# Kernel tuning notes

Measured on AMD Instinct MI355X. Metric: run time of the kernel, lower is better.

The kernel has to match this reference:

```python
import jax, jax.numpy as jnp
import numpy as np

# ROI Align config (module attributes in the original torch wrapper)
SPATIAL_SCALE = 0.25
POOLED_H = 7
POOLED_W = 7
SAMPLE_NUM = 2
ROI_END_MODE = 1  # Ascend: end coord gets +roi_end_mode before scaling


def setup_inputs() -> dict:
    key = jax.random.key(0)
    k_feat, k_b, k_xy, k_wh = jax.random.split(key, 4)
    B, C, H, W = 2, 256, 200, 200
    N = 1000
    feat = jax.random.normal(k_feat, (B, C, H, W), dtype=jnp.float32)
    img_h, img_w = H / SPATIAL_SCALE, W / SPATIAL_SCALE
    bidx = jax.random.randint(k_b, (N,), 0, B).astype(jnp.float32)
    xy = jax.random.uniform(k_xy, (N, 2), dtype=jnp.float32)
    wh = jax.random.uniform(k_wh, (N, 2), dtype=jnp.float32)
    x1 = xy[:, 0] * (img_w - 64.0)
    y1 = xy[:, 1] * (img_h - 64.0)
    x2 = x1 + 8.0 + wh[:, 0] * 200.0
    y2 = y1 + 8.0 + wh[:, 1] * 200.0
    rois = jnp.stack([bidx, x1, y1, x2, y2], axis=1)  # [N,5]
    return {"input": feat, "rois": rois}


def _axis_coords(start, bin_size, pooled, sn):
    # sample coord for grid index g: start + bin_size*(g+0.5)/sn, g in [0, pooled*sn)
    g = jnp.arange(pooled * sn, dtype=jnp.float32)
    return start[:, None] + bin_size[:, None] * (g[None, :] + 0.5) / sn  # [N, pooled*sn]


def _bilinear_1d(c, size):
    # returns (low_idx, high_idx, w_low, w_high, valid) for coordinate array c
    valid = (c >= -1.0) & (c <= size)
    cc = jnp.clip(c, 0.0, size - 1.0)
    lo = jnp.floor(cc).astype(jnp.int32)
    lo = jnp.clip(lo, 0, size - 1)
    hi = jnp.clip(lo + 1, 0, size - 1)
    frac = cc - lo.astype(jnp.float32)
    return lo, hi, 1.0 - frac, frac, valid


def roi_align(feat, rois):
    B, C, H, W = feat.shape
    N = rois.shape[0]
    bidx = rois[:, 0].astype(jnp.int32)
    off = float(ROI_END_MODE)
    x1 = rois[:, 1] * SPATIAL_SCALE
    y1 = rois[:, 2] * SPATIAL_SCALE
    x2 = (rois[:, 3] + off) * SPATIAL_SCALE
    y2 = (rois[:, 4] + off) * SPATIAL_SCALE
    roi_w = jnp.maximum(x2 - x1, 1.0)
    roi_h = jnp.maximum(y2 - y1, 1.0)
    bin_h = roi_h / POOLED_H
    bin_w = roi_w / POOLED_W

    ys = _axis_coords(y1, bin_h, POOLED_H, SAMPLE_NUM)  # [N, GY]
    xs = _axis_coords(x1, bin_w, POOLED_W, SAMPLE_NUM)  # [N, GX]
    yl, yh, wyl, wyh, vy = _bilinear_1d(ys, H)
    xl, xh, wxl, wxh, vx = _bilinear_1d(xs, W)

    b = bidx[:, None, None]

    def gather(yi, xi):
        # advanced indexing -> [N, GY, GX, C]
        return feat[b, :, yi[:, :, None], xi[:, None, :]]

    val = (wyl[:, :, None, None] * wxl[:, None, :, None] * gather(yl, xl)
           + wyl[:, :, None, None] * wxh[:, None, :, None] * gather(yl, xh)
           + wyh[:, :, None, None] * wxl[:, None, :, None] * gather(yh, xl)
           + wyh[:, :, None, None] * wxh[:, None, :, None] * gather(yh, xh))
    mask = (vy[:, :, None] & vx[:, None, :]).astype(val.dtype)[..., None]
    val = val * mask  # [N, GY, GX, C]

    # average pool over the SAMPLE_NUM x SAMPLE_NUM grid inside each bin
    val = val.reshape(N, POOLED_H, SAMPLE_NUM, POOLED_W, SAMPLE_NUM, C)
    out = val.mean(axis=(2, 4))  # [N, PH, PW, C]
    return jnp.transpose(out, (0, 3, 1, 2))  # [N, C, PH, PW]


def reference(input, rois):
    return roi_align(input, rois)
```

## Files before the change

kernel.cpp:

```cpp
#include <hip/hip_runtime.h>
#include <hip/hip_bf16.h>


constexpr int C_TOT  = 256;
constexpr int H_FEAT = 200;
constexpr int W_FEAT = 200;
constexpr int HW     = H_FEAT * W_FEAT;
constexpr int S_TOT  = 49;
constexpr size_t FEATT_BYTES = (size_t)2 * HW * C_TOT * sizeof(unsigned short);
constexpr int NXCD = 8;
constexpr int NBUCKET = 32;

__global__ __launch_bounds__(1024) void roi_bin_kernel(
    const float* __restrict__ rois, int* __restrict__ perm, int N)
{
    __shared__ int hist[NBUCKET];
    __shared__ int base[NBUCKET];
    __shared__ int cnt[NBUCKET];
    int t = threadIdx.x;

    if (t < NBUCKET) { hist[t] = 0; cnt[t] = 0; }
    __syncthreads();

    int bucket = -1;
    if (t < N) {
        const float* r = rois + (size_t)t * 5;
        int   b  = (int)r[0];
        float cx = (r[1] + r[3]) * 0.5f * 0.25f;
        float cy = (r[2] + r[4]) * 0.5f * 0.25f;
        int qx = min(max((int)(cx * (4.0f / 200.0f)), 0), 3);
        int qy = min(max((int)(cy * (4.0f / 200.0f)), 0), 3);
        bucket = ((b & 1) << 4) | (qy << 2) | qx;
        atomicAdd(&hist[bucket], 1);
    }
    __syncthreads();

    if (t == 0) {
        int acc = 0;
        for (int i = 0; i < NBUCKET; ++i) { base[i] = acc; acc += hist[i]; }
    }
    __syncthreads();

    if (t < N) {
        int pos = base[bucket] + atomicAdd(&cnt[bucket], 1);
        perm[pos] = t;
    }
}

__global__ __launch_bounds__(256) void nchw_to_nhwc_bf16_kernel(
    const float* __restrict__ feat,
    unsigned short* __restrict__ featT)
{
    __shared__ float tile[32][33];
    int tx = threadIdx.x;
    int ty = threadIdx.y;
    int s0 = blockIdx.x * 32;
    int c0 = blockIdx.y * 32;
    int b  = blockIdx.z;

    const float* src = feat + ((size_t)b * C_TOT) * HW;
    #pragma unroll
    for (int i = 0; i < 4; ++i) {
        int r = ty + i * 8;
        tile[r][tx] = src[(size_t)(c0 + r) * HW + (s0 + tx)];
    }
    __syncthreads();
    unsigned short* dst = featT + ((size_t)b * HW) * C_TOT;
    #pragma unroll
    for (int i = 0; i < 4; ++i) {
        int r = ty + i * 8;
        float x = tile[tx][r];
        unsigned int u = __float_as_uint(x);
        unsigned int rb = (u + 0x7fffu + ((u >> 16) & 1u)) >> 16;
        dst[(size_t)(s0 + r) * C_TOT + (c0 + tx)] = (unsigned short)rb;
    }
}

__global__ __launch_bounds__(512) void roi_align_nhwc_kernel(
    const unsigned short* __restrict__ featT,
    const float* __restrict__ rois,
    const int* __restrict__ perm,
    float* __restrict__ out,
    int N, int use_perm)
{
    __shared__ alignas(16) float tile[C_TOT * S_TOT];

    int n;
    if (use_perm) {
        int chunk = (N + NXCD - 1) / NXCD;
        int rank  = (blockIdx.x & (NXCD - 1)) * chunk + (blockIdx.x >> 3);
        if (rank >= N) rank = blockIdx.x;
        n = perm[rank];
    } else {
        n = blockIdx.x;
    }

    int tid  = threadIdx.x;
    int wave = tid >> 6;
    int lane = tid & 63;
    int half = lane >> 5;
    int li   = lane & 31;

    const float* r = rois + (size_t)n * 5;
    int   b  = (int)r[0];
    float x1 = r[1] * 0.25f;
    float y1 = r[2] * 0.25f;
    float x2 = (r[3] + 1.0f) * 0.25f;
    float y2 = (r[4] + 1.0f) * 0.25f;
    float bin_w = fmaxf(x2 - x1, 1.0f) * (1.0f / 7.0f);
    float bin_h = fmaxf(y2 - y1, 1.0f) * (1.0f / 7.0f);

    const unsigned short* fb = featT + (size_t)b * HW * C_TOT + li * 8;
    int xorsw = (li >> 2) & 7;

    for (int s = wave; s < S_TOT; s += 8) {
        int ph = s / 7;
        int pw = s - ph * 7;

        int   yoff[2][2];
        int   xoff[2][2];
        float wy[2][2], wx[2][2];
        #pragma unroll
        for (int i = 0; i < 2; ++i) {
            float gy  = (float)(2 * ph + i);
            float cy  = y1 + bin_h * ((gy + 0.5f) * 0.5f);
            bool  vy  = (cy >= -1.0f) && (cy <= (float)H_FEAT);
            float ccy = fminf(fmaxf(cy, 0.0f), (float)(H_FEAT - 1));
            int   ylo = (int)ccy;
            int   yhi = min(ylo + 1, H_FEAT - 1);
            float fy  = ccy - (float)ylo;
            yoff[i][0] = ylo * W_FEAT;
            yoff[i][1] = yhi * W_FEAT;
            wy[i][0] = vy ? (1.0f - fy) * 0.5f : 0.0f;
            wy[i][1] = vy ? fy * 0.5f          : 0.0f;

            float gx  = (float)(2 * pw + i);
            float cx  = x1 + bin_w * ((gx + 0.5f) * 0.5f);
            bool  vx  = (cx >= -1.0f) && (cx <= (float)W_FEAT);
            float ccx = fminf(fmaxf(cx, 0.0f), (float)(W_FEAT - 1));
            int   xlo = (int)ccx;
            int   xhi = min(xlo + 1, W_FEAT - 1);
            float fx  = ccx - (float)xlo;
            xoff[i][0] = xlo;
            xoff[i][1] = xhi;
            wx[i][0] = vx ? (1.0f - fx) * 0.5f : 0.0f;
            wx[i][1] = vx ? fx * 0.5f          : 0.0f;
        }

        float acc[8];
        #pragma unroll
        for (int j = 0; j < 8; ++j) acc[j] = 0.0f;

        #pragma unroll
        for (int iy = 0; iy < 2; ++iy)
        #pragma unroll
        for (int jy = 0; jy < 2; ++jy)
        #pragma unroll
        for (int ix = 0; ix < 2; ++ix) {
            int   pixA = yoff[iy][jy] + xoff[ix][0];
            int   pixB = yoff[iy][jy] + xoff[ix][1];
            float wA   = wy[iy][jy] * wx[ix][0];
            float wB   = wy[iy][jy] * wx[ix][1];
            int   pix  = half ? pixB : pixA;
            float w    = half ? wB   : wA;
            const uint4 v = *reinterpret_cast<const uint4*>(
                fb + (size_t)pix * C_TOT);
            unsigned int u;
            u = v.x;
            acc[0] = fmaf(w, __uint_as_float(u << 16),          acc[0]);
            acc[1] = fmaf(w, __uint_as_float(u & 0xffff0000u),  acc[1]);
            u = v.y;
            acc[2] = fmaf(w, __uint_as_float(u << 16),          acc[2]);
            acc[3] = fmaf(w, __uint_as_float(u & 0xffff0000u),  acc[3]);
            u = v.z;
            acc[4] = fmaf(w, __uint_as_float(u << 16),          acc[4]);
            acc[5] = fmaf(w, __uint_as_float(u & 0xffff0000u),  acc[5]);
            u = v.w;
            acc[6] = fmaf(w, __uint_as_float(u << 16),          acc[6]);
            acc[7] = fmaf(w, __uint_as_float(u & 0xffff0000u),  acc[7]);
        }

        #pragma unroll
        for (int j = 0; j < 8; ++j) {
            float sum = acc[j] + __shfl_xor(acc[j], 32);
            if (half == 0) {
                int slot_ch = li * 8 + (j ^ xorsw);
                tile[slot_ch * S_TOT + s] = sum;
            }
        }
    }
    __syncthreads();

    float4* o4 = reinterpret_cast<float4*>(out + (size_t)n * (C_TOT * S_TOT));
    constexpr int Q4 = C_TOT * S_TOT / 4;
    for (int q4 = tid; q4 < Q4; q4 += 512) {
        int q = q4 * 4;
        float4 val;
        float* vp = reinterpret_cast<float*>(&val);
        #pragma unroll
        for (int e = 0; e < 4; ++e) {
            int qq = q + e;
            int ch = qq / S_TOT;
            int ss = qq - ch * S_TOT;
            int slot_ch = (ch & ~7) | ((ch & 7) ^ ((ch >> 5) & 7));
            vp[e] = tile[slot_ch * S_TOT + ss];
        }
        o4[q4] = val;
    }
}

constexpr int CPT = 4;
constexpr int CG  = C_TOT / CPT;

__global__ __launch_bounds__(256) void roi_align_direct_kernel(
    const float* __restrict__ feat,
    const float* __restrict__ rois,
    float* __restrict__ out,
    int N)
{
    int t = blockIdx.x * 256 + threadIdx.x;
    int total = N * CG * S_TOT;
    if (t >= total) return;

    int s   = t % S_TOT;
    int rem = t / S_TOT;
    int c0  = rem % CG;
    int n   = rem / CG;
    int ph  = s / 7;
    int pw  = s - ph * 7;

    const float* r = rois + (size_t)n * 5;
    int   b  = (int)r[0];
    float x1 = r[1] * 0.25f;
    float y1 = r[2] * 0.25f;
    float x2 = (r[3] + 1.0f) * 0.25f;
    float y2 = (r[4] + 1.0f) * 0.25f;
    float bin_w = fmaxf(x2 - x1, 1.0f) * (1.0f / 7.0f);
    float bin_h = fmaxf(y2 - y1, 1.0f) * (1.0f / 7.0f);

    int   roff[2][2], coff[2][2];
    float wy[2][2], wx[2][2];
    #pragma unroll
    for (int i = 0; i < 2; ++i) {
        float gy  = (float)(2 * ph + i);
        float cy  = y1 + bin_h * ((gy + 0.5f) * 0.5f);
        bool  vy  = (cy >= -1.0f) && (cy <= (float)H_FEAT);
        float ccy = fminf(fmaxf(cy, 0.0f), (float)(H_FEAT - 1));
        int   ylo = (int)ccy;
        int   yhi = min(ylo + 1, H_FEAT - 1);
        float fy  = ccy - (float)ylo;
        roff[i][0] = ylo * W_FEAT;
        roff[i][1] = yhi * W_FEAT;
        wy[i][0] = vy ? (1.0f - fy) : 0.0f;
        wy[i][1] = vy ? fy          : 0.0f;

        float gx  = (float)(2 * pw + i);
        float cx  = x1 + bin_w * ((gx + 0.5f) * 0.5f);
        bool  vx  = (cx >= -1.0f) && (cx <= (float)W_FEAT);
        float ccx = fminf(fmaxf(cx, 0.0f), (float)(W_FEAT - 1));
        int   xlo = (int)ccx;
        int   xhi = min(xlo + 1, W_FEAT - 1);
        float fx  = ccx - (float)xlo;
        coff[i][0] = xlo;
        coff[i][1] = xhi;
        wx[i][0] = vx ? (1.0f - fx) : 0.0f;
        wx[i][1] = vx ? fx          : 0.0f;
    }

    float w16[16];
    int   o16[16];
    #pragma unroll
    for (int iy = 0; iy < 2; ++iy)
    #pragma unroll
    for (int ix = 0; ix < 2; ++ix)
    #pragma unroll
    for (int jy = 0; jy < 2; ++jy)
    #pragma unroll
    for (int jx = 0; jx < 2; ++jx) {
        int idx = ((iy * 2 + ix) * 2 + jy) * 2 + jx;
        w16[idx] = wy[iy][jy] * wx[ix][jx];
        o16[idx] = roff[iy][jy] + coff[ix][jx];
    }

    size_t base  = ((size_t)b * C_TOT + c0) * HW;
    size_t obase = (size_t)n * (C_TOT * S_TOT) + (size_t)c0 * S_TOT + s;

    #pragma unroll
    for (int k = 0; k < CPT; ++k) {
        const float* f = feat + base + (size_t)k * CG * HW;
        float acc = 0.0f;
        #pragma unroll
        for (int j = 0; j < 16; ++j)
            acc = fmaf(w16[j], f[o16[j]], acc);
        out[obase + (size_t)k * (CG * S_TOT)] = acc * 0.25f;
    }
}

extern "C" void kernel_launch(void* const* d_in, const int* in_sizes, int n_in,
                              void* d_out, int out_size, void* d_ws, size_t ws_size,
                              hipStream_t stream) {
    const float* feat = (const float*)d_in[0];
    const float* rois = (const float*)d_in[1];
    float* out = (float*)d_out;
    int N = in_sizes[1] / 5;

    size_t need = FEATT_BYTES + 4096;
    if (ws_size >= need) {
        unsigned short* featT = (unsigned short*)d_ws;
        int* perm = (int*)((char*)d_ws + FEATT_BYTES);
        int use_perm = (N <= 1024) ? 1 : 0;
        if (use_perm)
            roi_bin_kernel<<<1, 1024, 0, stream>>>(rois, perm, N);
        dim3 tgrid(HW / 32, C_TOT / 32, 2);
        dim3 tblk(32, 8);
        nchw_to_nhwc_bf16_kernel<<<tgrid, tblk, 0, stream>>>(feat, featT);
        roi_align_nhwc_kernel<<<N, 512, 0, stream>>>(featT, rois, perm, out, N, use_perm);
    } else {
        int total  = N * CG * S_TOT;
        int blocks = (total + 255) / 256;
        roi_align_direct_kernel<<<blocks, 256, 0, stream>>>(feat, rois, out, N);
    }
}
```

Before: 61.16 us.

## Use persistent ROI-align blocks pulling work from per-XCD atomic queues

Replaces the one-block-per-ROI launch with a persistent grid of up to 768 blocks. Each block reads its hardware XCD id and claims ROIs via atomic counters from per-XCD slices of the spatially sorted permutation, stealing from other XCDs once its own slice runs out. The bin ordering also changes to a Morton-like interleave so that ROIs sharing an XCD are spatially close, aiming for better L2 locality and load balance. In exchange it adds global atomics, an extra barrier per ROI, and a dependency on reading a hardware register for the XCD id.

```diff
diff --git a/kernel.cpp b/kernel.cpp
--- a/kernel.cpp
+++ b/kernel.cpp
@@ -10,9 +10,11 @@
 constexpr size_t FEATT_BYTES = (size_t)2 * HW * C_TOT * sizeof(unsigned short);
 constexpr int NXCD = 8;
 constexpr int NBUCKET = 32;
+#define XCC_GETREG_IMM 63508
 
 __global__ __launch_bounds__(1024) void roi_bin_kernel(
-    const float* __restrict__ rois, int* __restrict__ perm, int N)
+    const float* __restrict__ rois, int* __restrict__ perm,
+    int* __restrict__ qcnt, int N)
 {
     __shared__ int hist[NBUCKET];
     __shared__ int base[NBUCKET];
@@ -20,6 +22,7 @@
     int t = threadIdx.x;
 
     if (t < NBUCKET) { hist[t] = 0; cnt[t] = 0; }
+    if (t < NXCD + 1) qcnt[t] = 0;
     __syncthreads();
 
     int bucket = -1;
@@ -30,7 +33,8 @@
         float cy = (r[2] + r[4]) * 0.5f * 0.25f;
         int qx = min(max((int)(cx * (4.0f / 200.0f)), 0), 3);
         int qy = min(max((int)(cy * (4.0f / 200.0f)), 0), 3);
-        bucket = ((b & 1) << 4) | (qy << 2) | qx;
+        int m  = ((qy & 2) << 2) | ((qx & 2) << 1) | ((qy & 1) << 1) | (qx & 1);
+        bucket = ((b & 1) << 4) | m;
         atomicAdd(&hist[bucket], 1);
     }
     __syncthreads();
@@ -76,136 +80,151 @@
     }
 }
 
-__global__ __launch_bounds__(512) void roi_align_nhwc_kernel(
+__global__ __launch_bounds__(512) void roi_align_persistent_kernel(
     const unsigned short* __restrict__ featT,
     const float* __restrict__ rois,
     const int* __restrict__ perm,
+    int* __restrict__ qcnt,
     float* __restrict__ out,
-    int N, int use_perm)
+    int N)
 {
     __shared__ alignas(16) float tile[C_TOT * S_TOT];
-
-    int n;
-    if (use_perm) {
-        int chunk = (N + NXCD - 1) / NXCD;
-        int rank  = (blockIdx.x & (NXCD - 1)) * chunk + (blockIdx.x >> 3);
-        if (rank >= N) rank = blockIdx.x;
-        n = perm[rank];
-    } else {
-        n = blockIdx.x;
-    }
+    __shared__ int s_n;
 
     int tid  = threadIdx.x;
     int wave = tid >> 6;
     int lane = tid & 63;
     int half = lane >> 5;
     int li   = lane & 31;
-
-    const float* r = rois + (size_t)n * 5;
-    int   b  = (int)r[0];
-    float x1 = r[1] * 0.25f;
-    float y1 = r[2] * 0.25f;
-    float x2 = (r[3] + 1.0f) * 0.25f;
-    float y2 = (r[4] + 1.0f) * 0.25f;
-    float bin_w = fmaxf(x2 - x1, 1.0f) * (1.0f / 7.0f);
-    float bin_h = fmaxf(y2 - y1, 1.0f) * (1.0f / 7.0f);
-
-    const unsigned short* fb = featT + (size_t)b * HW * C_TOT + li * 8;
     int xorsw = (li >> 2) & 7;
 
-    for (int s = wave; s < S_TOT; s += 8) {
-        int ph = s / 7;
-        int pw = s - ph * 7;
-
-        int   yoff[2][2];
-        int   xoff[2][2];
-        float wy[2][2], wx[2][2];
-        #pragma unroll
-        for (int i = 0; i < 2; ++i) {
-            float gy  = (float)(2 * ph + i);
-            float cy  = y1 + bin_h * ((gy + 0.5f) * 0.5f);
-            bool  vy  = (cy >= -1.0f) && (cy <= (float)H_FEAT);
-            float ccy = fminf(fmaxf(cy, 0.0f), (float)(H_FEAT - 1));
-            int   ylo = (int)ccy;
-            int   yhi = min(ylo + 1, H_FEAT - 1);
-            float fy  = ccy - (float)ylo;
-            yoff[i][0] = ylo * W_FEAT;
-            yoff[i][1] = yhi * W_FEAT;
-            wy[i][0] = vy ? (1.0f - fy) * 0.5f : 0.0f;
-            wy[i][1] = vy ? fy * 0.5f          : 0.0f;
-
-            float gx  = (float)(2 * pw + i);
-            float cx  = x1 + bin_w * ((gx + 0.5f) * 0.5f);
-            bool  vx  = (cx >= -1.0f) && (cx <= (float)W_FEAT);
-            float ccx = fminf(fmaxf(cx, 0.0f), (float)(W_FEAT - 1));
-            int   xlo = (int)ccx;
-            int   xhi = min(xlo + 1, W_FEAT - 1);
-            float fx  = ccx - (float)xlo;
-            xoff[i][0] = xlo;
-            xoff[i][1] = xhi;
-            wx[i][0] = vx ? (1.0f - fx) * 0.5f : 0.0f;
-            wx[i][1] = vx ? fx * 0.5f          : 0.0f;
+    int q   = N >> 3;
+    int rem = N & 7;
+
+    while (true) {
+        __syncthreads();
+        if (tid == 0) {
+            int xcd = (int)(__builtin_amdgcn_s_getreg(XCC_GETREG_IMM) & 7u);
+            int got = -1;
+            #pragma unroll
+            for (int k = 0; k < NXCD; ++k) {
+                int x   = (xcd + k) & 7;
+                int sz  = q + (x < rem ? 1 : 0);
+                int off = x * q + min(x, rem);
+                int r   = atomicAdd(&qcnt[x], 1);
+                if (r < sz) { got = perm[off + r]; break; }
+            }
+            s_n = got;
         }
-
-        float acc[8];
-        #pragma unroll
-        for (int j = 0; j < 8; ++j) acc[j] = 0.0f;
-
-        #pragma unroll
-        for (int iy = 0; iy < 2; ++iy)
-        #pragma unroll
-        for (int jy = 0; jy < 2; ++jy)
-        #pragma unroll
-        for (int ix = 0; ix < 2; ++ix) {
-            int   pixA = yoff[iy][jy] + xoff[ix][0];
-            int   pixB = yoff[iy][jy] + xoff[ix][1];
-            float wA   = wy[iy][jy] * wx[ix][0];
-            float wB   = wy[iy][jy] * wx[ix][1];
-            int   pix  = half ? pixB : pixA;
-            float w    = half ? wB   : wA;
-            const uint4 v = *reinterpret_cast<const uint4*>(
-                fb + (size_t)pix * C_TOT);
-            unsigned int u;
-            u = v.x;
-            acc[0] = fmaf(w, __uint_as_float(u << 16),          acc[0]);
-            acc[1] = fmaf(w, __uint_as_float(u & 0xffff0000u),  acc[1]);
-            u = v.y;
-            acc[2] = fmaf(w, __uint_as_float(u << 16),          acc[2]);
-            acc[3] = fmaf(w, __uint_as_float(u & 0xffff0000u),  acc[3]);
-            u = v.z;
-            acc[4] = fmaf(w, __uint_as_float(u << 16),          acc[4]);
-            acc[5] = fmaf(w, __uint_as_float(u & 0xffff0000u),  acc[5]);
-            u = v.w;
-            acc[6] = fmaf(w, __uint_as_float(u << 16),          acc[6]);
-            acc[7] = fmaf(w, __uint_as_float(u & 0xffff0000u),  acc[7]);
+        __syncthreads();
+        int n = s_n;
+        if (n < 0) break;
+
+        const float* r = rois + (size_t)n * 5;
+        int   b  = (int)r[0];
+        float x1 = r[1] * 0.25f;
+        float y1 = r[2] * 0.25f;
+        float x2 = (r[3] + 1.0f) * 0.25f;
+        float y2 = (r[4] + 1.0f) * 0.25f;
+        float bin_w = fmaxf(x2 - x1, 1.0f) * (1.0f / 7.0f);
+        float bin_h = fmaxf(y2 - y1, 1.0f) * (1.0f / 7.0f);
+
+        const unsigned short* fb = featT + (size_t)b * HW * C_TOT + li * 8;
+
+        for (int s = wave; s < S_TOT; s += 8) {
+            int ph = s / 7;
+            int pw = s - ph * 7;
+
+            int   yoff[2][2];
+            int   xoff[2][2];
+            float wy[2][2], wx[2][2];
+            #pragma unroll
+            for (int i = 0; i < 2; ++i) {
+                float gy  = (float)(2 * ph + i);
+                float cy  = y1 + bin_h * ((gy + 0.5f) * 0.5f);
+                bool  vy  = (cy >= -1.0f) && (cy <= (float)H_FEAT);
+                float ccy = fminf(fmaxf(cy, 0.0f), (float)(H_FEAT - 1));
+                int   ylo = (int)ccy;
+                int   yhi = min(ylo + 1, H_FEAT - 1);
+                float fy  = ccy - (float)ylo;
+                yoff[i][0] = ylo * W_FEAT;
+                yoff[i][1] = yhi * W_FEAT;
+                wy[i][0] = vy ? (1.0f - fy) * 0.5f : 0.0f;
+                wy[i][1] = vy ? fy * 0.5f          : 0.0f;
+
+                float gx  = (float)(2 * pw + i);
+                float cx  = x1 + bin_w * ((gx + 0.5f) * 0.5f);
+                bool  vx  = (cx >= -1.0f) && (cx <= (float)W_FEAT);
+                float ccx = fminf(fmaxf(cx, 0.0f), (float)(W_FEAT - 1));
+                int   xlo = (int)ccx;
+                int   xhi = min(xlo + 1, W_FEAT - 1);
+                float fx  = ccx - (float)xlo;
+                xoff[i][0] = xlo;
+                xoff[i][1] = xhi;
+                wx[i][0] = vx ? (1.0f - fx) * 0.5f : 0.0f;
+                wx[i][1] = vx ? fx * 0.5f          : 0.0f;
+            }
+
+            float acc[8];
+            #pragma unroll
+            for (int j = 0; j < 8; ++j) acc[j] = 0.0f;
+
+            #pragma unroll
+            for (int iy = 0; iy < 2; ++iy)
+            #pragma unroll
+            for (int jy = 0; jy < 2; ++jy)
+            #pragma unroll
+            for (int ix = 0; ix < 2; ++ix) {
+                int   pixA = yoff[iy][jy] + xoff[ix][0];
+                int   pixB = yoff[iy][jy] + xoff[ix][1];
+                float wA   = wy[iy][jy] * wx[ix][0];
+                float wB   = wy[iy][jy] * wx[ix][1];
+                int   pix  = half ? pixB : pixA;
+                float w    = half ? wB   : wA;
+                const uint4 v = *reinterpret_cast<const uint4*>(
+                    fb + (size_t)pix * C_TOT);
+                unsigned int u;
+                u = v.x;
+                acc[0] = fmaf(w, __uint_as_float(u << 16),          acc[0]);
+                acc[1] = fmaf(w, __uint_as_float(u & 0xffff0000u),  acc[1]);
+                u = v.y;
+                acc[2] = fmaf(w, __uint_as_float(u << 16),          acc[2]);
+                acc[3] = fmaf(w, __uint_as_float(u & 0xffff0000u),  acc[3]);
+                u = v.z;
+                acc[4] = fmaf(w, __uint_as_float(u << 16),          acc[4]);
+                acc[5] = fmaf(w, __uint_as_float(u & 0xffff0000u),  acc[5]);
+                u = v.w;
+                acc[6] = fmaf(w, __uint_as_float(u << 16),          acc[6]);
+                acc[7] = fmaf(w, __uint_as_float(u & 0xffff0000u),  acc[7]);
+            }
+
+            #pragma unroll
+            for (int j = 0; j < 8; ++j) {
+                float sum = acc[j] + __shfl_xor(acc[j], 32);
+                if (half == 0) {
+                    int slot_ch = li * 8 + (j ^ xorsw);
+                    tile[slot_ch * S_TOT + s] = sum;
+                }
+            }
         }
-
-        #pragma unroll
-        for (int j = 0; j < 8; ++j) {
-            float sum = acc[j] + __shfl_xor(acc[j], 32);
-            if (half == 0) {
-                int slot_ch = li * 8 + (j ^ xorsw);
-                tile[slot_ch * S_TOT + s] = sum;
-            }
+        __syncthreads();
+
+        float4* o4 = reinterpret_cast<float4*>(out + (size_t)n * (C_TOT * S_TOT));
+        constexpr int Q4 = C_TOT * S_TOT / 4;
+        for (int q4 = tid; q4 < Q4; q4 += 512) {
+            int qq0 = q4 * 4;
+            float4 val;
+            float* vp = reinterpret_cast<float*>(&val);
+            #pragma unroll
+            for (int e = 0; e < 4; ++e) {
+                int qq = qq0 + e;
+                int ch = qq / S_TOT;
+                int ss = qq - ch * S_TOT;
+                int slot_ch = (ch & ~7) | ((ch & 7) ^ ((ch >> 5) & 7));
+                vp[e] = tile[slot_ch * S_TOT + ss];
+            }
+            o4[q4] = val;
         }
-    }
-    __syncthreads();
-
-    float4* o4 = reinterpret_cast<float4*>(out + (size_t)n * (C_TOT * S_TOT));
-    constexpr int Q4 = C_TOT * S_TOT / 4;
-    for (int q4 = tid; q4 < Q4; q4 += 512) {
-        int q = q4 * 4;
-        float4 val;
-        float* vp = reinterpret_cast<float*>(&val);
-        #pragma unroll
-        for (int e = 0; e < 4; ++e) {
-            int qq = q + e;
-            int ch = qq / S_TOT;
-            int ss = qq - ch * S_TOT;
-            int slot_ch = (ch & ~7) | ((ch & 7) ^ ((ch >> 5) & 7));
-            vp[e] = tile[slot_ch * S_TOT + ss];
-        }
-        o4[q4] = val;
     }
 }
 
@@ -304,17 +323,18 @@
     float* out = (float*)d_out;
     int N = in_sizes[1] / 5;
 
-    size_t need = FEATT_BYTES + 4096;
-    if (ws_size >= need) {
+    size_t need = FEATT_BYTES + 4096 + 64;
+    if (ws_size >= need && N <= 1024) {
         unsigned short* featT = (unsigned short*)d_ws;
         int* perm = (int*)((char*)d_ws + FEATT_BYTES);
-        int use_perm = (N <= 1024) ? 1 : 0;
-        if (use_perm)
-            roi_bin_kernel<<<1, 1024, 0, stream>>>(rois, perm, N);
+        int* qcnt = (int*)((char*)d_ws + FEATT_BYTES + 4096);
+        roi_bin_kernel<<<1, 1024, 0, stream>>>(rois, perm, qcnt, N);
         dim3 tgrid(HW / 32, C_TOT / 32, 2);
         dim3 tblk(32, 8);
         nchw_to_nhwc_bf16_kernel<<<tgrid, tblk, 0, stream>>>(feat, featT);
-        roi_align_nhwc_kernel<<<N, 512, 0, stream>>>(featT, rois, perm, out, N, use_perm);
+        int pgrid = min(768, N);
+        roi_align_persistent_kernel<<<pgrid, 512, 0, stream>>>(
+            featT, rois, perm, qcnt, out, N);
     } else {
         int total  = N * CG * S_TOT;
         int blocks = (total + 255) / 256;
```

Measured after the change: 125.7 us. +105.6%, slower.

## Fuse transpose and ROI align into one persistent kernel with readiness flags

Applied to the files above, without the earlier changes.

Merges the NCHW-to-NHWC bf16 transpose and the ROI-align gather into a single kernel. The first blocks to arrive (by atomic ticket) transpose row stripes and bump per-batch, per-row-group counters; every block then pulls ROIs from an atomic work queue ordered by lowest row extent and spins until the row groups it needs are done. The aim is to overlap the transpose with the gather and drop a kernel launch and the full dependency barrier between them. The cost is spin-waiting, atomic overhead, and reliance on the transpose blocks being resident so the spin cannot deadlock.

```diff
diff --git a/kernel.cpp b/kernel.cpp
--- a/kernel.cpp
+++ b/kernel.cpp
@@ -1,5 +1,4 @@
 #include <hip/hip_runtime.h>
-#include <hip/hip_bf16.h>
 
 
 constexpr int C_TOT  = 256;
@@ -8,11 +7,27 @@
 constexpr int HW     = H_FEAT * W_FEAT;
 constexpr int S_TOT  = 49;
 constexpr size_t FEATT_BYTES = (size_t)2 * HW * C_TOT * sizeof(unsigned short);
-constexpr int NXCD = 8;
+constexpr int NT      = 320;
+constexpr int NSTRIPE = 2500;
 constexpr int NBUCKET = 32;
 
+__device__ __forceinline__ int gsize(int g) { return g == 3 ? 50 : 400; }
+
+__device__ __forceinline__ unsigned short bf16rne(float x) {
+    unsigned int u = __float_as_uint(x);
+    return (unsigned short)((u + 0x7fffu + ((u >> 16) & 1u)) >> 16);
+}
+
+__device__ __forceinline__ int roi_yhi(const float* r) {
+    float y1c = r[2] * 0.25f;
+    float y2c = (r[4] + 1.0f) * 0.25f;
+    float ye  = y1c + fmaxf(y2c - y1c, 1.0f);
+    return min(199, (int)fmaxf(ye, 0.0f) + 1);
+}
+
 __global__ __launch_bounds__(1024) void roi_bin_kernel(
-    const float* __restrict__ rois, int* __restrict__ perm, int N)
+    const float* __restrict__ rois, int* __restrict__ perm,
+    int* __restrict__ qbase, int N)
 {
     __shared__ int hist[NBUCKET];
     __shared__ int base[NBUCKET];
@@ -20,188 +35,320 @@
     int t = threadIdx.x;
 
     if (t < NBUCKET) { hist[t] = 0; cnt[t] = 0; }
+    if (t < 160) qbase[t] = 0;
     __syncthreads();
 
     int bucket = -1;
     if (t < N) {
         const float* r = rois + (size_t)t * 5;
-        int   b  = (int)r[0];
-        float cx = (r[1] + r[3]) * 0.5f * 0.25f;
-        float cy = (r[2] + r[4]) * 0.5f * 0.25f;
-        int qx = min(max((int)(cx * (4.0f / 200.0f)), 0), 3);
-        int qy = min(max((int)(cy * (4.0f / 200.0f)), 0), 3);
-        bucket = ((b & 1) << 4) | (qy << 2) | qx;
+        int b    = (int)r[0];
+        int yh   = roi_yhi(r);
+        bucket   = ((b & 1) << 4) | min(15, yh >> 4);
         atomicAdd(&hist[bucket], 1);
     }
     __syncthreads();
-
     if (t == 0) {
         int acc = 0;
         for (int i = 0; i < NBUCKET; ++i) { base[i] = acc; acc += hist[i]; }
     }
     __syncthreads();
-
     if (t < N) {
         int pos = base[bucket] + atomicAdd(&cnt[bucket], 1);
         perm[pos] = t;
     }
 }
 
-__global__ __launch_bounds__(256) void nchw_to_nhwc_bf16_kernel(
+__global__ __launch_bounds__(512) void roi_align_fused_kernel(
     const float* __restrict__ feat,
-    unsigned short* __restrict__ featT)
-{
-    __shared__ float tile[32][33];
-    int tx = threadIdx.x;
-    int ty = threadIdx.y;
-    int s0 = blockIdx.x * 32;
-    int c0 = blockIdx.y * 32;
-    int b  = blockIdx.z;
-
-    const float* src = feat + ((size_t)b * C_TOT) * HW;
-    #pragma unroll
-    for (int i = 0; i < 4; ++i) {
-        int r = ty + i * 8;
-        tile[r][tx] = src[(size_t)(c0 + r) * HW + (s0 + tx)];
-    }
-    __syncthreads();
-    unsigned short* dst = featT + ((size_t)b * HW) * C_TOT;
-    #pragma unroll
-    for (int i = 0; i < 4; ++i) {
-        int r = ty + i * 8;
-        float x = tile[tx][r];
-        unsigned int u = __float_as_uint(x);
-        unsigned int rb = (u + 0x7fffu + ((u >> 16) & 1u)) >> 16;
-        dst[(size_t)(s0 + r) * C_TOT + (c0 + tx)] = (unsigned short)rb;
-    }
-}
-
-__global__ __launch_bounds__(512) void roi_align_nhwc_kernel(
-    const unsigned short* __restrict__ featT,
+    unsigned short* __restrict__ featT,
     const float* __restrict__ rois,
     const int* __restrict__ perm,
+    int* __restrict__ qbase,
     float* __restrict__ out,
-    int N, int use_perm)
+    int N)
 {
-    __shared__ alignas(16) float tile[C_TOT * S_TOT];
-
-    int n;
-    if (use_perm) {
-        int chunk = (N + NXCD - 1) / NXCD;
-        int rank  = (blockIdx.x & (NXCD - 1)) * chunk + (blockIdx.x >> 3);
-        if (rank >= N) rank = blockIdx.x;
-        n = perm[rank];
-    } else {
-        n = blockIdx.x;
-    }
+    __shared__ alignas(16) float smem[C_TOT * S_TOT];
+    __shared__ int s_role, s_r;
 
     int tid  = threadIdx.x;
     int wave = tid >> 6;
     int lane = tid & 63;
     int half = lane >> 5;
     int li   = lane & 31;
+    int xorsw = (li >> 2) & 7;
+
+    if (tid == 0) s_role = atomicAdd(&qbase[128], 1);
+    __syncthreads();
+    int role = s_role;
+
+    if (role < NT) {
+        float (*tt)[32][33] = reinterpret_cast<float(*)[32][33]>(smem);
+        int tx  = tid & 31;
+        int tyw = (tid >> 5) & 7;
+        int ti  = tid >> 8;
+        for (int st = role; st < NSTRIPE; st += NT) {
+            int b   = st >= 1250 ? 1 : 0;
+            int sg  = st - b * 1250;
+            int sp0 = sg * 32;
+            const float* src = feat + (size_t)b * C_TOT * HW;
+            unsigned short* dst = featT + (size_t)b * HW * C_TOT;
+            #pragma unroll
+            for (int ct = 0; ct < 4; ++ct) {
+                int cb = (ct * 2 + ti) * 32;
+                #pragma unroll
+                for (int i = 0; i < 4; ++i) {
+                    int r = tyw + i * 8;
+                    tt[ti][r][tx] = src[(size_t)(cb + r) * HW + sp0 + tx];
+                }
+                __syncthreads();
+                #pragma unroll
+                for (int i = 0; i < 4; ++i) {
+                    int r = tyw + i * 8;
+                    dst[(size_t)(sp0 + r) * C_TOT + cb + tx] = bf16rne(tt[ti][tx][r]);
+                }
+                __syncthreads();
+            }
+            if (tid == 0) {
+                __threadfence();
+                int g = sg < 400 ? 0 : sg < 800 ? 1 : sg < 1200 ? 2 : 3;
+                atomicAdd(&qbase[(b * 4 + g) * 16], 1);
+            }
+        }
+    }
+
+    while (true) {
+        __syncthreads();
+        if (tid == 0) s_r = atomicAdd(&qbase[144], 1);
+        __syncthreads();
+        int rk = s_r;
+        if (rk >= N) break;
+        int n = perm[rk];
+
+        const float* r = rois + (size_t)n * 5;
+        int   b  = (int)r[0];
+        float x1 = r[1] * 0.25f;
+        float y1 = r[2] * 0.25f;
+        float x2 = (r[3] + 1.0f) * 0.25f;
+        float y2 = (r[4] + 1.0f) * 0.25f;
+        float bin_w = fmaxf(x2 - x1, 1.0f) * (1.0f / 7.0f);
+        float bin_h = fmaxf(y2 - y1, 1.0f) * (1.0f / 7.0f);
+
+        if (tid == 0) {
+            int gw = min(3, roi_yhi(r) >> 6);
+            for (int g = 0; g <= gw; ++g) {
+                while (__hip_atomic_load(&qbase[(b * 4 + g) * 16],
+                                         __ATOMIC_RELAXED,
+                                         __HIP_MEMORY_SCOPE_AGENT) < gsize(g))
+                    __builtin_amdgcn_s_sleep(16);
+            }
+        }
+        __syncthreads();
+
+        const unsigned short* fb = featT + (size_t)b * HW * C_TOT + li * 8;
+
+        for (int s = wave; s < S_TOT; s += 8) {
+            int ph = s / 7;
+            int pw = s - ph * 7;
+
+            int   yoff[2][2], xoff[2][2];
+            float wy[2][2], wx[2][2];
+            #pragma unroll
+            for (int i = 0; i < 2; ++i) {
+                float gy  = (float)(2 * ph + i);
+                float cy  = y1 + bin_h * ((gy + 0.5f) * 0.5f);
+                bool  vy  = (cy >= -1.0f) && (cy <= (float)H_FEAT);
+                float ccy = fminf(fmaxf(cy, 0.0f), (float)(H_FEAT - 1));
+                int   ylo = (int)ccy;
+                int   yhi = min(ylo + 1, H_FEAT - 1);
+                float fy  = ccy - (float)ylo;
+                yoff[i][0] = ylo * W_FEAT;
+                yoff[i][1] = yhi * W_FEAT;
+                wy[i][0] = vy ? (1.0f - fy) * 0.5f : 0.0f;
+                wy[i][1] = vy ? fy * 0.5f          : 0.0f;
+
+                float gx  = (float)(2 * pw + i);
+                float cx  = x1 + bin_w * ((gx + 0.5f) * 0.5f);
+                bool  vx  = (cx >= -1.0f) && (cx <= (float)W_FEAT);
+                float ccx = fminf(fmaxf(cx, 0.0f), (float)(W_FEAT - 1));
+                int   xlo = (int)ccx;
+                int   xhi = min(xlo + 1, W_FEAT - 1);
+                float fx  = ccx - (float)xlo;
+                xoff[i][0] = xlo;
+                xoff[i][1] = xhi;
+                wx[i][0] = vx ? (1.0f - fx) * 0.5f : 0.0f;
+                wx[i][1] = vx ? fx * 0.5f          : 0.0f;
+            }
+
+            float acc[8];
+            #pragma unroll
+            for (int j = 0; j < 8; ++j) acc[j] = 0.0f;
+
+            #pragma unroll
+            for (int iy = 0; iy < 2; ++iy)
+            #pragma unroll
+            for (int jy = 0; jy < 2; ++jy)
+            #pragma unroll
+            for (int ix = 0; ix < 2; ++ix) {
+                int   pixA = yoff[iy][jy] + xoff[ix][0];
+                int   pixB = yoff[iy][jy] + xoff[ix][1];
+                float wA   = wy[iy][jy] * wx[ix][0];
+                float wB   = wy[iy][jy] * wx[ix][1];
+                int   pix  = half ? pixB : pixA;
+                float w    = half ? wB   : wA;
+                const uint4 v = *reinterpret_cast<const uint4*>(
+                    fb + (size_t)pix * C_TOT);
+                unsigned int u;
+                u = v.x;
+                acc[0] = fmaf(w, __uint_as_float(u << 16),         acc[0]);
+                acc[1] = fmaf(w, __uint_as_float(u & 0xffff0000u), acc[1]);
+                u = v.y;
+                acc[2] = fmaf(w, __uint_as_float(u << 16),         acc[2]);
+                acc[3] = fmaf(w, __uint_as_float(u & 0xffff0000u), acc[3]);
+                u = v.z;
+                acc[4] = fmaf(w, __uint_as_float(u << 16),         acc[4]);
+                acc[5] = fmaf(w, __uint_as_float(u & 0xffff0000u), acc[5]);
+                u = v.w;
+                acc[6] = fmaf(w, __uint_as_float(u << 16),         acc[6]);
+                acc[7] = fmaf(w, __uint_as_float(u & 0xffff0000u), acc[7]);
+            }
+
+            #pragma unroll
+            for (int j = 0; j < 8; ++j) {
+                float sum = acc[j] + __shfl_xor(acc[j], 32);
+                if (half == 0) {
+                    int slot_ch = li * 8 + (j ^ xorsw);
+                    smem[slot_ch * S_TOT + s] = sum;
+                }
+            }
+        }
+        __syncthreads();
+
+        float4* o4 = reinterpret_cast<float4*>(out + (size_t)n * (C_TOT * S_TOT));
+        constexpr int Q4 = C_TOT * S_TOT / 4;
+        for (int q4 = tid; q4 < Q4; q4 += 512) {
+            int qq0 = q4 * 4;
+            float4 val;
+            float* vp = reinterpret_cast<float*>(&val);
+            #pragma unroll
+            for (int e = 0; e < 4; ++e) {
+                int qq = qq0 + e;
+                int ch = qq / S_TOT;
+                int ss = qq - ch * S_TOT;
+                int slot_ch = (ch & ~7) | ((ch & 7) ^ ((ch >> 5) & 7));
+                vp[e] = smem[slot_ch * S_TOT + ss];
+            }
+            o4[q4] = val;
+        }
+    }
+}
+
+__global__ __launch_bounds__(256) void nchw_to_nhwc_bf16_kernel(
+    const float* __restrict__ feat, unsigned short* __restrict__ featT)
+{
+    __shared__ float tile[32][33];
+    int tx = threadIdx.x, ty = threadIdx.y;
+    int s0 = blockIdx.x * 32, c0 = blockIdx.y * 32, b = blockIdx.z;
+    const float* src = feat + ((size_t)b * C_TOT) * HW;
+    #pragma unroll
+    for (int i = 0; i < 4; ++i) {
+        int r = ty + i * 8;
+        tile[r][tx] = src[(size_t)(c0 + r) * HW + (s0 + tx)];
+    }
+    __syncthreads();
+    unsigned short* dst = featT + ((size_t)b * HW) * C_TOT;
+    #pragma unroll
+    for (int i = 0; i < 4; ++i) {
+        int r = ty + i * 8;
+        dst[(size_t)(s0 + r) * C_TOT + (c0 + tx)] = bf16rne(tile[tx][r]);
+    }
+}
+
+__global__ __launch_bounds__(512) void roi_align_nhwc_kernel(
+    const unsigned short* __restrict__ featT,
+    const float* __restrict__ rois,
+    float* __restrict__ out, int N)
+{
+    __shared__ alignas(16) float tile[C_TOT * S_TOT];
+    int n = blockIdx.x;
+    int tid = threadIdx.x, wave = tid >> 6, lane = tid & 63;
+    int half = lane >> 5, li = lane & 31, xorsw = (li >> 2) & 7;
 
     const float* r = rois + (size_t)n * 5;
     int   b  = (int)r[0];
-    float x1 = r[1] * 0.25f;
-    float y1 = r[2] * 0.25f;
-    float x2 = (r[3] + 1.0f) * 0.25f;
-    float y2 = (r[4] + 1.0f) * 0.25f;
+    float x1 = r[1] * 0.25f, y1 = r[2] * 0.25f;
+    float x2 = (r[3] + 1.0f) * 0.25f, y2 = (r[4] + 1.0f) * 0.25f;
     float bin_w = fmaxf(x2 - x1, 1.0f) * (1.0f / 7.0f);
     float bin_h = fmaxf(y2 - y1, 1.0f) * (1.0f / 7.0f);
-
     const unsigned short* fb = featT + (size_t)b * HW * C_TOT + li * 8;
-    int xorsw = (li >> 2) & 7;
 
     for (int s = wave; s < S_TOT; s += 8) {
-        int ph = s / 7;
-        int pw = s - ph * 7;
-
-        int   yoff[2][2];
-        int   xoff[2][2];
+        int ph = s / 7, pw = s - ph * 7;
+        int yoff[2][2], xoff[2][2];
         float wy[2][2], wx[2][2];
         #pragma unroll
         for (int i = 0; i < 2; ++i) {
-            float gy  = (float)(2 * ph + i);
-            float cy  = y1 + bin_h * ((gy + 0.5f) * 0.5f);
-            bool  vy  = (cy >= -1.0f) && (cy <= (float)H_FEAT);
+            float gy = (float)(2 * ph + i);
+            float cy = y1 + bin_h * ((gy + 0.5f) * 0.5f);
+            bool  vy = (cy >= -1.0f) && (cy <= (float)H_FEAT);
             float ccy = fminf(fmaxf(cy, 0.0f), (float)(H_FEAT - 1));
-            int   ylo = (int)ccy;
-            int   yhi = min(ylo + 1, H_FEAT - 1);
-            float fy  = ccy - (float)ylo;
-            yoff[i][0] = ylo * W_FEAT;
-            yoff[i][1] = yhi * W_FEAT;
+            int ylo = (int)ccy, yhi = min(ylo + 1, H_FEAT - 1);
+            float fy = ccy - (float)ylo;
+            yoff[i][0] = ylo * W_FEAT; yoff[i][1] = yhi * W_FEAT;
             wy[i][0] = vy ? (1.0f - fy) * 0.5f : 0.0f;
             wy[i][1] = vy ? fy * 0.5f          : 0.0f;
-
-            float gx  = (float)(2 * pw + i);
-            float cx  = x1 + bin_w * ((gx + 0.5f) * 0.5f);
-            bool  vx  = (cx >= -1.0f) && (cx <= (float)W_FEAT);
+            float gx = (float)(2 * pw + i);
+            float cx = x1 + bin_w * ((gx + 0.5f) * 0.5f);
+            bool  vx = (cx >= -1.0f) && (cx <= (float)W_FEAT);
             float ccx = fminf(fmaxf(cx, 0.0f), (float)(W_FEAT - 1));
-            int   xlo = (int)ccx;
-            int   xhi = min(xlo + 1, W_FEAT - 1);
-            float fx  = ccx - (float)xlo;
-            xoff[i][0] = xlo;
-            xoff[i][1] = xhi;
+            int xlo = (int)ccx, xhi = min(xlo + 1, W_FEAT - 1);
+            float fx = ccx - (float)xlo;
+            xoff[i][0] = xlo; xoff[i][1] = xhi;
             wx[i][0] = vx ? (1.0f - fx) * 0.5f : 0.0f;
             wx[i][1] = vx ? fx * 0.5f          : 0.0f;
         }
-
         float acc[8];
         #pragma unroll
         for (int j = 0; j < 8; ++j) acc[j] = 0.0f;
-
         #pragma unroll
         for (int iy = 0; iy < 2; ++iy)
         #pragma unroll
         for (int jy = 0; jy < 2; ++jy)
         #pragma unroll
         for (int ix = 0; ix < 2; ++ix) {
-            int   pixA = yoff[iy][jy] + xoff[ix][0];
-            int   pixB = yoff[iy][jy] + xoff[ix][1];
-            float wA   = wy[iy][jy] * wx[ix][0];
-            float wB   = wy[iy][jy] * wx[ix][1];
-            int   pix  = half ? pixB : pixA;
-            float w    = half ? wB   : wA;
-            const uint4 v = *reinterpret_cast<const uint4*>(
-                fb + (size_t)pix * C_TOT);
+            int pixA = yoff[iy][jy] + xoff[ix][0];
+            int pixB = yoff[iy][jy] + xoff[ix][1];
+            float wA = wy[iy][jy] * wx[ix][0];
+            float wB = wy[iy][jy] * wx[ix][1];
+            int pix = half ? pixB : pixA;
+            float w = half ? wB : wA;
+            const uint4 v = *reinterpret_cast<const uint4*>(fb + (size_t)pix * C_TOT);
             unsigned int u;
-            u = v.x;
-            acc[0] = fmaf(w, __uint_as_float(u << 16),          acc[0]);
-            acc[1] = fmaf(w, __uint_as_float(u & 0xffff0000u),  acc[1]);
-            u = v.y;
-            acc[2] = fmaf(w, __uint_as_float(u << 16),          acc[2]);
-            acc[3] = fmaf(w, __uint_as_float(u & 0xffff0000u),  acc[3]);
-            u = v.z;
-            acc[4] = fmaf(w, __uint_as_float(u << 16),          acc[4]);
-            acc[5] = fmaf(w, __uint_as_float(u & 0xffff0000u),  acc[5]);
-            u = v.w;
-            acc[6] = fmaf(w, __uint_as_float(u << 16),          acc[6]);
-            acc[7] = fmaf(w, __uint_as_float(u & 0xffff0000u),  acc[7]);
-        }
-
+            u = v.x; acc[0] = fmaf(w, __uint_as_float(u << 16), acc[0]);
+                     acc[1] = fmaf(w, __uint_as_float(u & 0xffff0000u), acc[1]);
+            u = v.y; acc[2] = fmaf(w, __uint_as_float(u << 16), acc[2]);
+                     acc[3] = fmaf(w, __uint_as_float(u & 0xffff0000u), acc[3]);
+            u = v.z; acc[4] = fmaf(w, __uint_as_float(u << 16), acc[4]);
+                     acc[5] = fmaf(w, __uint_as_float(u & 0xffff0000u), acc[5]);
+            u = v.w; acc[6] = fmaf(w, __uint_as_float(u << 16), acc[6]);
+                     acc[7] = fmaf(w, __uint_as_float(u & 0xffff0000u), acc[7]);
+        }
         #pragma unroll
         for (int j = 0; j < 8; ++j) {
             float sum = acc[j] + __shfl_xor(acc[j], 32);
-            if (half == 0) {
-                int slot_ch = li * 8 + (j ^ xorsw);
-                tile[slot_ch * S_TOT + s] = sum;
-            }
-        }
-    }
-    __syncthreads();
-
+            if (half == 0) tile[(li * 8 + (j ^ xorsw)) * S_TOT + s] = sum;
+        }
+    }
+    __syncthreads();
     float4* o4 = reinterpret_cast<float4*>(out + (size_t)n * (C_TOT * S_TOT));
     constexpr int Q4 = C_TOT * S_TOT / 4;
     for (int q4 = tid; q4 < Q4; q4 += 512) {
-        int q = q4 * 4;
+        int qq0 = q4 * 4;
         float4 val;
         float* vp = reinterpret_cast<float*>(&val);
         #pragma unroll
         for (int e = 0; e < 4; ++e) {
-            int qq = q + e;
-            int ch = qq / S_TOT;
-            int ss = qq - ch * S_TOT;
+            int qq = qq0 + e;
+            int ch = qq / S_TOT, ss = qq - ch * S_TOT;
             int slot_ch = (ch & ~7) | ((ch & 7) ^ ((ch >> 5) & 7));
             vp[e] = tile[slot_ch * S_TOT + ss];
         }
@@ -213,62 +360,44 @@
 constexpr int CG  = C_TOT / CPT;
 
 __global__ __launch_bounds__(256) void roi_align_direct_kernel(
-    const float* __restrict__ feat,
-    const float* __restrict__ rois,
-    float* __restrict__ out,
-    int N)
+    const float* __restrict__ feat, const float* __restrict__ rois,
+    float* __restrict__ out, int N)
 {
     int t = blockIdx.x * 256 + threadIdx.x;
     int total = N * CG * S_TOT;
     if (t >= total) return;
-
-    int s   = t % S_TOT;
-    int rem = t / S_TOT;
-    int c0  = rem % CG;
-    int n   = rem / CG;
-    int ph  = s / 7;
-    int pw  = s - ph * 7;
-
+    int s = t % S_TOT, rem = t / S_TOT, c0 = rem % CG, n = rem / CG;
+    int ph = s / 7, pw = s - ph * 7;
     const float* r = rois + (size_t)n * 5;
     int   b  = (int)r[0];
-    float x1 = r[1] * 0.25f;
-    float y1 = r[2] * 0.25f;
-    float x2 = (r[3] + 1.0f) * 0.25f;
-    float y2 = (r[4] + 1.0f) * 0.25f;
+    float x1 = r[1] * 0.25f, y1 = r[2] * 0.25f;
+    float x2 = (r[3] + 1.0f) * 0.25f, y2 = (r[4] + 1.0f) * 0.25f;
     float bin_w = fmaxf(x2 - x1, 1.0f) * (1.0f / 7.0f);
     float bin_h = fmaxf(y2 - y1, 1.0f) * (1.0f / 7.0f);
-
-    int   roff[2][2], coff[2][2];
+    int roff[2][2], coff[2][2];
     float wy[2][2], wx[2][2];
     #pragma unroll
     for (int i = 0; i < 2; ++i) {
-        float gy  = (float)(2 * ph + i);
-        float cy  = y1 + bin_h * ((gy + 0.5f) * 0.5f);
-        bool  vy  = (cy >= -1.0f) && (cy <= (float)H_FEAT);
+        float gy = (float)(2 * ph + i);
+        float cy = y1 + bin_h * ((gy + 0.5f) * 0.5f);
+        bool  vy = (cy >= -1.0f) && (cy <= (float)H_FEAT);
         float ccy = fminf(fmaxf(cy, 0.0f), (float)(H_FEAT - 1));
-        int   ylo = (int)ccy;
-        int   yhi = min(ylo + 1, H_FEAT - 1);
-        float fy  = ccy - (float)ylo;
-        roff[i][0] = ylo * W_FEAT;
-        roff[i][1] = yhi * W_FEAT;
+        int ylo = (int)ccy, yhi = min(ylo + 1, H_FEAT - 1);
+        float fy = ccy - (float)ylo;
+        roff[i][0] = ylo * W_FEAT; roff[i][1] = yhi * W_FEAT;
         wy[i][0] = vy ? (1.0f - fy) : 0.0f;
         wy[i][1] = vy ? fy          : 0.0f;
-
-        float gx  = (float)(2 * pw + i);
-        float cx  = x1 + bin_w * ((gx + 0.5f) * 0.5f);
-        bool  vx  = (cx >= -1.0f) && (cx <= (float)W_FEAT);
+        float gx = (float)(2 * pw + i);
+        float cx = x1 + bin_w * ((gx + 0.5f) * 0.5f);
+        bool  vx = (cx >= -1.0f) && (cx <= (float)W_FEAT);
         float ccx = fminf(fmaxf(cx, 0.0f), (float)(W_FEAT - 1));
-        int   xlo = (int)ccx;
-        int   xhi = min(xlo + 1, W_FEAT - 1);
-        float fx  = ccx - (float)xlo;
-        coff[i][0] = xlo;
-        coff[i][1] = xhi;
+        int xlo = (int)ccx, xhi = min(xlo + 1, W_FEAT - 1);
+        float fx = ccx - (float)xlo;
+        coff[i][0] = xlo; coff[i][1] = xhi;
         wx[i][0] = vx ? (1.0f - fx) : 0.0f;
         wx[i][1] = vx ? fx          : 0.0f;
     }
-
-    float w16[16];
-    int   o16[16];
+    float w16[16]; int o16[16];
     #pragma unroll
     for (int iy = 0; iy < 2; ++iy)
     #pragma unroll
@@ -281,10 +410,8 @@
         w16[idx] = wy[iy][jy] * wx[ix][jx];
         o16[idx] = roff[iy][jy] + coff[ix][jx];
     }
-
     size_t base  = ((size_t)b * C_TOT + c0) * HW;
     size_t obase = (size_t)n * (C_TOT * S_TOT) + (size_t)c0 * S_TOT + s;
-
     #pragma unroll
     for (int k = 0; k < CPT; ++k) {
         const float* f = feat + base + (size_t)k * CG * HW;
@@ -304,17 +431,20 @@
     float* out = (float*)d_out;
     int N = in_sizes[1] / 5;
 
-    size_t need = FEATT_BYTES + 4096;
-    if (ws_size >= need) {
+    size_t need = FEATT_BYTES + 4096 + 1024;
+    if (ws_size >= need && N >= 512 && N <= 1024) {
         unsigned short* featT = (unsigned short*)d_ws;
-        int* perm = (int*)((char*)d_ws + FEATT_BYTES);
-        int use_perm = (N <= 1024) ? 1 : 0;
-        if (use_perm)
-            roi_bin_kernel<<<1, 1024, 0, stream>>>(rois, perm, N);
+        int* perm  = (int*)((char*)d_ws + FEATT_BYTES);
+        int* qbase = (int*)((char*)d_ws + FEATT_BYTES + 4096);
+        roi_bin_kernel<<<1, 1024, 0, stream>>>(rois, perm, qbase, N);
+        roi_align_fused_kernel<<<N, 512, 0, stream>>>(
+            feat, featT, rois, perm, qbase, out, N);
+    } else if (ws_size >= need && N <= 1024) {
+        unsigned short* featT = (unsigned short*)d_ws;
         dim3 tgrid(HW / 32, C_TOT / 32, 2);
         dim3 tblk(32, 8);
         nchw_to_nhwc_bf16_kernel<<<tgrid, tblk, 0, stream>>>(feat, featT);
-        roi_align_nhwc_kernel<<<N, 512, 0, stream>>>(featT, rois, perm, out, N, use_perm);
+        roi_align_nhwc_kernel<<<N, 512, 0, stream>>>(featT, rois, out, N);
     } else {
         int total  = N * CG * S_TOT;
         int blocks = (total + 255) / 256;
```

Result: slower. 209.0 us (+241.7%).
